# Kernel optimization log

Hardware: AMD Instinct MI355X
Metric: run time of the kernel (lower is better)

## Reference

```python
import jax, jax.numpy as jnp
import numpy as np
from math import exp, log

# Instant-NGP style multi-hash-grid constants (match init_kwargs)
BASE_RES = 16
MAX_RES = 2048
N_GRIDS = 16
LOG2_T = 19
TABLE_SIZE = 1 << LOG2_T  # power of two -> mod == low-bit mask
FEAT = 2
N_POINTS = 1_000_000

_pls = exp((log(MAX_RES) - log(BASE_RES)) / (N_GRIDS - 1))
RESOLUTIONS = np.floor(np.array([BASE_RES * _pls ** i for i in range(N_GRIDS)])).astype(np.float32)
# 8 voxel corner offsets, i-major (i*4 + j*2 + k) like the torch VOXEL_VTX_OFFSET
OFFSETS = np.array([[i, j, k] for i in (0, 1) for j in (0, 1) for k in (0, 1)], dtype=np.int32)
PRIMES = np.array([1, 2654435761, 805459861], dtype=np.uint32)


def setup_inputs() -> dict:
    key = jax.random.key(0)
    k1, k2 = jax.random.split(key)
    x = jax.random.normal(k1, (N_POINTS, 3), dtype=jnp.float32)
    # nn.init.uniform_(weight, a=-1e-4, b=1e-4)
    tables = jax.random.uniform(k2, (N_GRIDS, TABLE_SIZE, FEAT),
                                minval=-1e-4, maxval=1e-4, dtype=jnp.float32)
    return {"x": x, "tables": tables}


def _forward(x, tables):
    inbox = jnp.all((x >= -1.0) & (x <= 1.0), axis=-1)  # [B]
    offs = jnp.asarray(OFFSETS)                          # [8,3]
    primes = jnp.asarray(PRIMES)                         # [3] uint32
    res = jnp.asarray(RESOLUTIONS)                       # [G]
    # torch computes x_normed / interp weights under no_grad -> no grad to x
    xs = jax.lax.stop_gradient(x)

    def level(table, r):
        # (x - bbox_min) / (bbox_max - bbox_min) * resolution, bbox = [-1,1]^3
        xn = (xs + 1.0) * 0.5 * r                        # [B,3]
        v0 = jnp.floor(xn).astype(jnp.int32)             # [B,3]
        w = xn - v0.astype(jnp.float32)                  # [B,3] trilerp weights
        vidx = (v0[:, None, :] + offs[None]).astype(jnp.uint32)  # [B,8,3]
        # prime-XOR spatial hash; uint32 wraparound matches torch int64 math
        # modulo the power-of-two table size (low bits identical)
        h = (vidx[..., 0] * primes[0]) ^ (vidx[..., 1] * primes[1]) ^ (vidx[..., 2] * primes[2])
        h = (h & jnp.uint32(TABLE_SIZE - 1)).astype(jnp.int32)   # [B,8]
        feats = table[h]                                  # [B,8,F] gather
        # corner (i,j,k) weight = prod over dims of (w if bit else 1-w)
        wgt = jnp.prod(jnp.where(offs[None] == 1, w[:, None, :], 1.0 - w[:, None, :]), axis=-1)  # [B,8]
        c = jnp.einsum('bc,bcf->bf', wgt, feats)          # [B,F]
        return jnp.where(inbox[:, None], c, 0.0)          # out-of-bbox -> zeros

    per_level = jax.vmap(level)(tables, res)              # [G,B,F]
    B = x.shape[0]
    return jnp.transpose(per_level, (1, 0, 2)).reshape(B, N_GRIDS * FEAT)


def reference(x, tables):
    return _forward(x, tables)
```

## Files before the change

kernel.cpp:

```cpp
#include <hip/hip_runtime.h>
#include <hip/hip_bf16.h>
#include <math.h>

#define N_POINTS 1000000
#define N_GRIDS  16
#define LOG2_T   19
#define TABLE_MASK ((1u << LOG2_T) - 1u)
#define NBLOCKS  ((N_POINTS + 255) / 256)
#define CONV_BLOCKS 4096
#define FUSED_BLOCKS 2048
#define TAILB_BLOCKS 4096
#define N_ENTRIES (N_GRIDS << LOG2_T)
#define NCELL_AX 32
#define N_CELLS  (NCELL_AX * NCELL_AX * NCELL_AX)

struct ResArr { float r[N_GRIDS]; };

__device__ __forceinline__ unsigned pack_bf16x2(float a, float b)
{
    __hip_bfloat16 ha = __float2bfloat16(a);
    __hip_bfloat16 hb = __float2bfloat16(b);
    unsigned short ua = *(unsigned short*)&ha;
    unsigned short ub = *(unsigned short*)&hb;
    return (unsigned)ua | ((unsigned)ub << 16);
}

__device__ __forceinline__ float2 unpack_bf16x2(unsigned v)
{
    unsigned lo = (v & 0xffffu) << 16;
    unsigned hi = v & 0xffff0000u;
    return make_float2(__uint_as_float(lo), __uint_as_float(hi));
}

__device__ __forceinline__ unsigned expand_bits(unsigned v)
{
    v &= 0x3ffu;
    v = (v | (v << 16)) & 0x30000FFu;
    v = (v | (v << 8))  & 0x300F00Fu;
    v = (v | (v << 4))  & 0x30C30C3u;
    v = (v | (v << 2))  & 0x9249249u;
    return v;
}

__device__ __forceinline__ int morton_cell(float x0, float x1, float x2)
{
    int cx = (int)floorf((x0 + 1.f) * 16.f);
    int cy = (int)floorf((x1 + 1.f) * 16.f);
    int cz = (int)floorf((x2 + 1.f) * 16.f);
    cx = min(NCELL_AX - 1, max(0, cx));
    cy = min(NCELL_AX - 1, max(0, cy));
    cz = min(NCELL_AX - 1, max(0, cz));
    return (int)((expand_bits((unsigned)cx) << 2) |
                 (expand_bits((unsigned)cy) << 1) |
                  expand_bits((unsigned)cz));
}

__device__ __forceinline__ void gather_level_bf16(
    float x0, float x1, float x2, float r,
    const unsigned* __restrict__ tbl, float& c0, float& c1)
{
    const float xn0 = (x0 + 1.0f) * 0.5f * r;
    const float xn1 = (x1 + 1.0f) * 0.5f * r;
    const float xn2 = (x2 + 1.0f) * 0.5f * r;
    const float f0 = floorf(xn0), f1 = floorf(xn1), f2 = floorf(xn2);
    const unsigned v0 = (unsigned)(int)f0;
    const unsigned v1 = (unsigned)(int)f1;
    const unsigned v2 = (unsigned)(int)f2;
    const float w0 = xn0 - f0, w1 = xn1 - f1, w2 = xn2 - f2;
    const unsigned d = v0 ^ (v0 + 1u);

    unsigned sa4[4];
    uint2    pa[4];
    #pragma unroll
    for (int yz = 0; yz < 4; ++yz) {
        const unsigned vy = v1 + ((yz >> 1) & 1);
        const unsigned vz = v2 + (yz & 1);
        const unsigned m  = (vy * 2654435761u) ^ (vz * 805459861u);
        const unsigned sa = (v0 ^ m) & TABLE_MASK;
        sa4[yz] = sa;
        pa[yz]  = ((const uint2*)tbl)[sa >> 1];
    }
    const bool paired = (d == 1u);
    unsigned ub[4];
    #pragma unroll
    for (int yz = 0; yz < 4; ++yz) {
        unsigned u = 0;
        if (!paired) u = tbl[(sa4[yz] ^ d) & TABLE_MASK];
        ub[yz] = u;
    }

    unsigned fv[8];
    #pragma unroll
    for (int yz = 0; yz < 4; ++yz) {
        const unsigned odd = sa4[yz] & 1u;
        const unsigned uA = odd ? pa[yz].y : pa[yz].x;
        const unsigned uB = paired ? (odd ? pa[yz].x : pa[yz].y)
                                   : ub[yz];
        fv[yz]     = uA;
        fv[4 + yz] = uB;
    }

    c0 = 0.f; c1 = 0.f;
    #pragma unroll
    for (int k = 0; k < 8; ++k) {
        const float wgt = ((k & 4) ? w0 : 1.0f - w0) *
                          ((k & 2) ? w1 : 1.0f - w1) *
                          ((k & 1) ? w2 : 1.0f - w2);
        const float2 f = unpack_bf16x2(fv[k]);
        c0 += wgt * f.x;
        c1 += wgt * f.y;
    }
}

__global__ __launch_bounds__(256)
void hist_kernel(const float* __restrict__ x, int* __restrict__ rank,
                 unsigned* __restrict__ hist)
{
    const int p = blockIdx.x * 256 + threadIdx.x;
    if (p >= N_POINTS) return;
    const float x0 = x[3 * p], x1 = x[3 * p + 1], x2 = x[3 * p + 2];
    const bool inbox = (x0 >= -1.f) & (x0 <= 1.f) &
                       (x1 >= -1.f) & (x1 <= 1.f) &
                       (x2 >= -1.f) & (x2 <= 1.f);
    if (inbox) {
        const int cell = morton_cell(x0, x1, x2);
        atomicAdd(&hist[cell], 1u);
        rank[p] = cell;
    } else {
        rank[p] = -1;
    }
}

__global__ __launch_bounds__(1024)
void scan_kernel(unsigned* __restrict__ hist, unsigned* __restrict__ counter)
{
    __shared__ unsigned partial[1024];
    const int tid = threadIdx.x;
    uint4* __restrict__ hp = (uint4*)hist + tid * 8;
    uint4 vv[8];
    unsigned s = 0;
    #pragma unroll
    for (int i = 0; i < 8; ++i) {
        vv[i] = hp[i];
        s += vv[i].x + vv[i].y + vv[i].z + vv[i].w;
    }
    partial[tid] = s;
    __syncthreads();
    for (int off = 1; off < 1024; off <<= 1) {
        unsigned t = (tid >= off) ? partial[tid - off] : 0u;
        __syncthreads();
        partial[tid] += t;
        __syncthreads();
    }
    if (tid == 1023) counter[0] = partial[1023];
    unsigned run = partial[tid] - s;
    #pragma unroll
    for (int i = 0; i < 8; ++i) {
        uint4 o;
        o.x = run; run += vv[i].x;
        o.y = run; run += vv[i].y;
        o.z = run; run += vv[i].z;
        o.w = run; run += vv[i].w;
        hp[i] = o;
    }
}

__global__ __launch_bounds__(256)
void scatter_conv_kernel(const float* __restrict__ tables,
                         unsigned* __restrict__ tb,
                         const float* __restrict__ x, int* __restrict__ rank,
                         float4* __restrict__ xw, unsigned* __restrict__ hist)
{
    if (blockIdx.x < CONV_BLOCKS) {
        const unsigned nthr = CONV_BLOCKS * 256;
        for (unsigned e4 = blockIdx.x * 256 + threadIdx.x; e4 < (N_ENTRIES / 4);
             e4 += nthr) {
            const float4 a = ((const float4*)tables)[2 * e4];
            const float4 b = ((const float4*)tables)[2 * e4 + 1];
            uint4 o;
            o.x = pack_bf16x2(a.x, a.y);
            o.y = pack_bf16x2(a.z, a.w);
            o.z = pack_bf16x2(b.x, b.y);
            o.w = pack_bf16x2(b.z, b.w);
            ((uint4*)tb)[e4] = o;
        }
    } else {
        const int p = (blockIdx.x - CONV_BLOCKS) * 256 + threadIdx.x;
        if (p >= N_POINTS) return;
        const int cell = rank[p];
        if (cell < 0) return;
        const unsigned rk = atomicAdd(&hist[cell], 1u);
        rank[p] = (int)rk;
        xw[rk] = make_float4(x[3 * p], x[3 * p + 1], x[3 * p + 2],
                             __int_as_float(p));
    }
}

__global__ __launch_bounds__(256)
void fused_levels_kernel(const float4* __restrict__ xw,
                         const unsigned* __restrict__ counter,
                         const unsigned* __restrict__ tb,
                         unsigned* __restrict__ ws2, ResArr res)
{
    const unsigned k    = blockIdx.x & 7;
    const unsigned bix  = blockIdx.x >> 3;
    const unsigned nbx  = gridDim.x >> 3;
    const unsigned cnt  = *counter;
    const unsigned per  = (cnt + nbx - 1) / nbx;
    const unsigned lo   = bix * per;
    const unsigned hi   = min(cnt, lo + per);

    #pragma unroll 1
    for (int t = 0; t < 2; ++t) {
        const int g = t ? (15 - (int)k) : (int)k;
        const float r = res.r[g];
        const unsigned* __restrict__ tbl = tb + ((size_t)g << LOG2_T);
        unsigned* __restrict__ wrow = ws2 + (size_t)g * N_POINTS;
        for (unsigned i = lo + threadIdx.x; i < hi; i += 256) {
            const float4 v = xw[i];
            float c0, c1;
            gather_level_bf16(v.x, v.y, v.z, r, tbl, c0, c1);
            wrow[i] = pack_bf16x2(c0, c1);
        }
    }
}

__global__ __launch_bounds__(256)
void tail_kernel(const int* __restrict__ rank, const float4* __restrict__ xw,
                 const unsigned* __restrict__ counter,
                 const unsigned* __restrict__ ws2, float* __restrict__ out)
{
    const int t = threadIdx.x;
    if (blockIdx.x < NBLOCKS) {
        const int P0 = blockIdx.x * 256;
        float4* __restrict__ out4 = (float4*)out + (size_t)P0 * 8;
        const float4 z = make_float4(0.f, 0.f, 0.f, 0.f);
        #pragma unroll
        for (int i = 0; i < 8; ++i) {
            const int j  = i * 256 + t;
            const int pp = P0 + (j >> 3);
            if (pp < N_POINTS && rank[pp] < 0) out4[j] = z;
        }
    } else {
        const unsigned cnt = *counter;
        const unsigned tot = cnt * 8u;
        const unsigned bix = blockIdx.x - NBLOCKS;
        for (unsigned tg = bix * 256 + t; tg < tot; tg += TAILB_BLOCKS * 256) {
            const unsigned i = tg >> 3, q = tg & 7;
            const unsigned a = ws2[(size_t)(2 * q) * N_POINTS + i];
            const unsigned b = ws2[(size_t)(2 * q + 1) * N_POINTS + i];
            const int p = __float_as_int(xw[i].w);
            const float2 fa = unpack_bf16x2(a);
            const float2 fb = unpack_bf16x2(b);
            ((float4*)out)[(size_t)p * 8 + q] =
                make_float4(fa.x, fa.y, fb.x, fb.y);
        }
    }
}

__device__ __forceinline__ void gather_level_f32(
    float x0, float x1, float x2, float r,
    const float2* __restrict__ tbl, float& c0, float& c1)
{
    const float xn0 = (x0 + 1.0f) * 0.5f * r;
    const float xn1 = (x1 + 1.0f) * 0.5f * r;
    const float xn2 = (x2 + 1.0f) * 0.5f * r;
    const float f0 = floorf(xn0), f1 = floorf(xn1), f2 = floorf(xn2);
    const unsigned v0 = (unsigned)(int)f0;
    const unsigned v1 = (unsigned)(int)f1;
    const unsigned v2 = (unsigned)(int)f2;
    const float w0 = xn0 - f0, w1 = xn1 - f1, w2 = xn2 - f2;
    c0 = 0.f; c1 = 0.f;
    #pragma unroll
    for (int k = 0; k < 8; ++k) {
        const unsigned vx = v0 + ((k >> 2) & 1);
        const unsigned vy = v1 + ((k >> 1) & 1);
        const unsigned vz = v2 + (k & 1);
        unsigned h = (vx * 1u) ^ (vy * 2654435761u) ^ (vz * 805459861u);
        h &= TABLE_MASK;
        const float wgt = ((k & 4) ? w0 : 1.0f - w0) *
                          ((k & 2) ? w1 : 1.0f - w1) *
                          ((k & 1) ? w2 : 1.0f - w2);
        const float2 f = tbl[h];
        c0 += wgt * f.x;
        c1 += wgt * f.y;
    }
}

__global__ __launch_bounds__(256)
void mono_kernel(const float* __restrict__ x, const float* __restrict__ tables,
                 float* __restrict__ out, ResArr res)
{
    int idx = blockIdx.x * blockDim.x + threadIdx.x;
    if (idx >= N_POINTS * N_GRIDS) return;
    int b = idx >> 4, g = idx & 15;
    float x0 = x[b * 3], x1 = x[b * 3 + 1], x2 = x[b * 3 + 2];
    bool inbox = (x0 >= -1.f) & (x0 <= 1.f) & (x1 >= -1.f) & (x1 <= 1.f) &
                 (x2 >= -1.f) & (x2 <= 1.f);
    float c0 = 0.f, c1 = 0.f;
    if (inbox) {
        const float2* tbl = (const float2*)tables + ((size_t)g << LOG2_T);
        gather_level_f32(x0, x1, x2, res.r[g], tbl, c0, c1);
    }
    ((float2*)out)[(size_t)b * N_GRIDS + g] = make_float2(c0, c1);
}

extern "C" void kernel_launch(void* const* d_in, const int* in_sizes, int n_in,
                              void* d_out, int out_size, void* d_ws, size_t ws_size,
                              hipStream_t stream)
{
    const float* x      = (const float*)d_in[0];
    const float* tables = (const float*)d_in[1];
    float* out          = (float*)d_out;

    ResArr res;
    double pls = exp((log(2048.0) - log(16.0)) / 15.0);
    for (int i = 0; i < N_GRIDS; ++i)
        res.r[i] = (float)floor(16.0 * pow(pls, (double)i));

    const size_t off_hist = 256;
    const size_t off_rank = off_hist + (size_t)N_CELLS * 4;
    const size_t off_xw   = off_rank + (size_t)N_POINTS * 4;
    const size_t off_ws2  = off_xw + (size_t)N_POINTS * 16;
    const size_t off_tb   = off_ws2 + (size_t)N_GRIDS * N_POINTS * 4;
    const size_t ws_needed = off_tb + (size_t)N_ENTRIES * 4;

    if (ws_size < ws_needed) {
        int total = N_POINTS * N_GRIDS;
        mono_kernel<<<(total + 255) / 256, 256, 0, stream>>>(x, tables, out, res);
        return;
    }

    char* w = (char*)d_ws;
    unsigned* counter = (unsigned*)w;
    unsigned* hist    = (unsigned*)(w + off_hist);
    int*      rank    = (int*)(w + off_rank);
    float4*   xw      = (float4*)(w + off_xw);
    unsigned* ws2     = (unsigned*)(w + off_ws2);
    unsigned* tb      = (unsigned*)(w + off_tb);

    (void)hipMemsetAsync(w, 0, off_rank, stream);
    hist_kernel<<<NBLOCKS, 256, 0, stream>>>(x, rank, hist);
    scan_kernel<<<1, 1024, 0, stream>>>(hist, counter);
    scatter_conv_kernel<<<CONV_BLOCKS + NBLOCKS, 256, 0, stream>>>(
        tables, tb, x, rank, xw, hist);
    fused_levels_kernel<<<FUSED_BLOCKS, 256, 0, stream>>>(xw, counter, tb,
                                                          ws2, res);
    tail_kernel<<<NBLOCKS + TAILB_BLOCKS, 256, 0, stream>>>(rank, xw, counter,
                                                            ws2, out);
}
```

Baseline: 177.7 us.

## Widen hash-grid corner loads to 16B and move out-of-box zeroing into hist kernel

The bf16 gather now loads an aligned 4-entry (uint4) group instead of a pair, so the x-neighbour corner is served from the same load whenever the two hash slots differ only in the low two bits. A separate scalar load is issued only when they do not. Zero-filling of out-of-box output rows moves from the tail kernel into hist_kernel, so the tail no longer re-reads rank or launches the extra zeroing blocks, and the unused rank write-back in the scatter kernel is removed. The wider loads fetch more bytes per gather, and hist_kernel now does scattered 128B row writes.

```diff
diff --git a/kernel.cpp b/kernel.cpp
--- a/kernel.cpp
+++ b/kernel.cpp
@@ -55,6 +55,13 @@
                   expand_bits((unsigned)cz));
 }
 
+__device__ __forceinline__ unsigned sel4(uint4 P, unsigned idx)
+{
+    const unsigned lo = (idx & 1u) ? P.y : P.x;
+    const unsigned hi = (idx & 1u) ? P.w : P.z;
+    return (idx & 2u) ? hi : lo;
+}
+
 __device__ __forceinline__ void gather_level_bf16(
     float x0, float x1, float x2, float r,
     const unsigned* __restrict__ tbl, float& c0, float& c1)
@@ -70,7 +77,7 @@
     const unsigned d = v0 ^ (v0 + 1u);
 
     unsigned sa4[4];
-    uint2    pa[4];
+    uint4    pa[4];
     #pragma unroll
     for (int yz = 0; yz < 4; ++yz) {
         const unsigned vy = v1 + ((yz >> 1) & 1);
@@ -78,24 +85,24 @@
         const unsigned m  = (vy * 2654435761u) ^ (vz * 805459861u);
         const unsigned sa = (v0 ^ m) & TABLE_MASK;
         sa4[yz] = sa;
-        pa[yz]  = ((const uint2*)tbl)[sa >> 1];
-    }
-    const bool paired = (d == 1u);
+        pa[yz]  = ((const uint4*)tbl)[sa >> 2];
+    }
+    const bool far = (d > 3u);
     unsigned ub[4];
     #pragma unroll
     for (int yz = 0; yz < 4; ++yz) {
         unsigned u = 0;
-        if (!paired) u = tbl[(sa4[yz] ^ d) & TABLE_MASK];
+        if (far) u = tbl[(sa4[yz] ^ d) & TABLE_MASK];
         ub[yz] = u;
     }
 
     unsigned fv[8];
     #pragma unroll
     for (int yz = 0; yz < 4; ++yz) {
-        const unsigned odd = sa4[yz] & 1u;
-        const unsigned uA = odd ? pa[yz].y : pa[yz].x;
-        const unsigned uB = paired ? (odd ? pa[yz].x : pa[yz].y)
-                                   : ub[yz];
+        const unsigned ia = sa4[yz] & 3u;
+        const unsigned ib = (sa4[yz] ^ d) & 3u;
+        const unsigned uA = sel4(pa[yz], ia);
+        const unsigned uB = far ? ub[yz] : sel4(pa[yz], ib);
         fv[yz]     = uA;
         fv[4 + yz] = uB;
     }
@@ -114,7 +121,7 @@
 
 __global__ __launch_bounds__(256)
 void hist_kernel(const float* __restrict__ x, int* __restrict__ rank,
-                 unsigned* __restrict__ hist)
+                 unsigned* __restrict__ hist, float* __restrict__ out)
 {
     const int p = blockIdx.x * 256 + threadIdx.x;
     if (p >= N_POINTS) return;
@@ -128,6 +135,10 @@
         rank[p] = cell;
     } else {
         rank[p] = -1;
+        float4* __restrict__ row = (float4*)out + (size_t)p * 8;
+        const float4 z = make_float4(0.f, 0.f, 0.f, 0.f);
+        #pragma unroll
+        for (int i = 0; i < 8; ++i) row[i] = z;
     }
 }
 
@@ -168,7 +179,8 @@
 __global__ __launch_bounds__(256)
 void scatter_conv_kernel(const float* __restrict__ tables,
                          unsigned* __restrict__ tb,
-                         const float* __restrict__ x, int* __restrict__ rank,
+                         const float* __restrict__ x,
+                         const int* __restrict__ rank,
                          float4* __restrict__ xw, unsigned* __restrict__ hist)
 {
     if (blockIdx.x < CONV_BLOCKS) {
@@ -190,7 +202,6 @@
         const int cell = rank[p];
         if (cell < 0) return;
         const unsigned rk = atomicAdd(&hist[cell], 1u);
-        rank[p] = (int)rk;
         xw[rk] = make_float4(x[3 * p], x[3 * p + 1], x[3 * p + 2],
                              __int_as_float(p));
     }
@@ -226,35 +237,23 @@
 }
 
 __global__ __launch_bounds__(256)
-void tail_kernel(const int* __restrict__ rank, const float4* __restrict__ xw,
+void tail_kernel(const float4* __restrict__ xw,
                  const unsigned* __restrict__ counter,
                  const unsigned* __restrict__ ws2, float* __restrict__ out)
 {
     const int t = threadIdx.x;
-    if (blockIdx.x < NBLOCKS) {
-        const int P0 = blockIdx.x * 256;
-        float4* __restrict__ out4 = (float4*)out + (size_t)P0 * 8;
-        const float4 z = make_float4(0.f, 0.f, 0.f, 0.f);
-        #pragma unroll
-        for (int i = 0; i < 8; ++i) {
-            const int j  = i * 256 + t;
-            const int pp = P0 + (j >> 3);
-            if (pp < N_POINTS && rank[pp] < 0) out4[j] = z;
-        }
-    } else {
-        const unsigned cnt = *counter;
-        const unsigned tot = cnt * 8u;
-        const unsigned bix = blockIdx.x - NBLOCKS;
-        for (unsigned tg = bix * 256 + t; tg < tot; tg += TAILB_BLOCKS * 256) {
-            const unsigned i = tg >> 3, q = tg & 7;
-            const unsigned a = ws2[(size_t)(2 * q) * N_POINTS + i];
-            const unsigned b = ws2[(size_t)(2 * q + 1) * N_POINTS + i];
-            const int p = __float_as_int(xw[i].w);
-            const float2 fa = unpack_bf16x2(a);
-            const float2 fb = unpack_bf16x2(b);
-            ((float4*)out)[(size_t)p * 8 + q] =
-                make_float4(fa.x, fa.y, fb.x, fb.y);
-        }
+    const unsigned cnt = *counter;
+    const unsigned tot = cnt * 8u;
+    for (unsigned tg = blockIdx.x * 256 + t; tg < tot;
+         tg += TAILB_BLOCKS * 256) {
+        const unsigned i = tg >> 3, q = tg & 7;
+        const unsigned a = ws2[(size_t)(2 * q) * N_POINTS + i];
+        const unsigned b = ws2[(size_t)(2 * q + 1) * N_POINTS + i];
+        const int p = __float_as_int(xw[i].w);
+        const float2 fa = unpack_bf16x2(a);
+        const float2 fb = unpack_bf16x2(b);
+        ((float4*)out)[(size_t)p * 8 + q] =
+            make_float4(fa.x, fa.y, fb.x, fb.y);
     }
 }
 
@@ -340,12 +339,11 @@
     unsigned* tb      = (unsigned*)(w + off_tb);
 
     (void)hipMemsetAsync(w, 0, off_rank, stream);
-    hist_kernel<<<NBLOCKS, 256, 0, stream>>>(x, rank, hist);
+    hist_kernel<<<NBLOCKS, 256, 0, stream>>>(x, rank, hist, out);
     scan_kernel<<<1, 1024, 0, stream>>>(hist, counter);
     scatter_conv_kernel<<<CONV_BLOCKS + NBLOCKS, 256, 0, stream>>>(
         tables, tb, x, rank, xw, hist);
     fused_levels_kernel<<<FUSED_BLOCKS, 256, 0, stream>>>(xw, counter, tb,
                                                           ws2, res);
-    tail_kernel<<<NBLOCKS + TAILB_BLOCKS, 256, 0, stream>>>(rank, xw, counter,
-                                                            ws2, out);
-}
+    tail_kernel<<<TAILB_BLOCKS, 256, 0, stream>>>(xw, counter, ws2, out);
+}
```

Measured after the change: 172.2 us. 3.1% less time.
